# Kernel optimization log

Measured on AMD Instinct MI355X. Metric: run time of the kernel, lower is better.

## Reference

```python
import jax, jax.numpy as jnp
import numpy as np

B, S, H, UNITS = 32, 2048, 1024, 1024

def setup_inputs() -> dict:
    key = jax.random.key(0)
    ks = jax.random.split(key, 8)
    sc_h = 1.0 / np.sqrt(H)
    sc_u = 1.0 / np.sqrt(UNITS)
    return {
        "query": jax.random.normal(ks[0], (B, H), jnp.float32),
        "values": jax.random.normal(ks[1], (B, S, H), jnp.float32),
        "W1": jax.random.normal(ks[2], (H, UNITS), jnp.float32) * sc_h,
        "b1": jnp.zeros((UNITS,), jnp.float32),
        "W2": jax.random.normal(ks[3], (H, UNITS), jnp.float32) * sc_h,
        "b2": jnp.zeros((UNITS,), jnp.float32),
        "V": jax.random.normal(ks[4], (UNITS, 1), jnp.float32) * sc_u,
        "bv": jnp.zeros((1,), jnp.float32),
    }

def reference(query, values, W1, b1, W2, b2, V, bv):
    # W1(values): [B,S,U]; W2(query)[:,None,:]: [B,1,U] broadcast-added
    proj = jnp.tanh(
        jnp.einsum("bsh,hu->bsu", values, W1) + b1
        + (query @ W2 + b2)[:, None, :]
    )
    score = proj @ V + bv                      # [B,S,1]
    attention_weights = jax.nn.softmax(score, axis=1)  # softmax over seq
    context_vector = jnp.sum(attention_weights * values, axis=1)  # [B,H]
    return context_vector, attention_weights
```

## Files before the change

### kernel.cpp

```cpp
#include <hip/hip_runtime.h>
#include <hip/hip_bf16.h>


#define B_ 32
#define S_ 2048
#define H_ 1024
#define U_ 1024
#define M_ (B_ * S_)

typedef __bf16 bf16;
typedef __bf16 bf16x8 __attribute__((ext_vector_type(8)));
typedef __bf16 bf16x4 __attribute__((ext_vector_type(4)));
typedef float  f32x4  __attribute__((ext_vector_type(4)));

__device__ __forceinline__ void gl2lds16(const void* g, void* l) {
    __builtin_amdgcn_global_load_lds(
        (const __attribute__((address_space(1))) void*)g,
        (__attribute__((address_space(3))) void*)l, 16, 0, 0);
}

__global__ void cast_values(const float* __restrict__ in, bf16* __restrict__ out) {
    long i = ((long)blockIdx.x * 256 + threadIdx.x) * 8;
    float4 f0 = *reinterpret_cast<const float4*>(in + i);
    float4 f1 = *reinterpret_cast<const float4*>(in + i + 4);
    bf16x8 o;
    o[0] = (bf16)f0.x; o[1] = (bf16)f0.y; o[2] = (bf16)f0.z; o[3] = (bf16)f0.w;
    o[4] = (bf16)f1.x; o[5] = (bf16)f1.y; o[6] = (bf16)f1.z; o[7] = (bf16)f1.w;
    *reinterpret_cast<bf16x8*>(out + i) = o;
}

__global__ void transpose_w1(const float* __restrict__ W1, bf16* __restrict__ W1T) {
    __shared__ bf16 t[64 * 65];
    int h0 = blockIdx.x * 64, u0 = blockIdx.y * 64;
    int tid = threadIdx.x;
    #pragma unroll
    for (int i = 0; i < 16; ++i) {
        int idx = i * 256 + tid;
        int r = idx >> 6, c = idx & 63;
        t[c * 65 + r] = (bf16)W1[(long)(h0 + r) * U_ + u0 + c];
    }
    __syncthreads();
    #pragma unroll
    for (int i = 0; i < 16; ++i) {
        int idx = i * 256 + tid;
        int r = idx >> 6, c = idx & 63;
        W1T[(long)(u0 + r) * H_ + h0 + c] = t[r * 65 + c];
    }
}

__global__ void q2_kernel(const float* __restrict__ query, const float* __restrict__ W2,
                          const float* __restrict__ b2, float* __restrict__ q2) {
    __shared__ float qsh[H_];
    __shared__ float part[4][64];
    int b = blockIdx.y;
    int u0 = blockIdx.x * 64;
    int tid = threadIdx.x;
    int ul = tid & 63, kc = tid >> 6;
    for (int i = tid; i < H_; i += 256) qsh[i] = query[b * H_ + i];
    __syncthreads();
    float acc = 0.f;
    const float* wp = W2 + (long)(kc * 256) * U_ + u0 + ul;
    #pragma unroll 8
    for (int h = 0; h < 256; ++h) acc += qsh[kc * 256 + h] * wp[(long)h * U_];
    part[kc][ul] = acc;
    __syncthreads();
    if (tid < 64)
        q2[b * U_ + u0 + tid] = part[0][tid] + part[1][tid] + part[2][tid] + part[3][tid]
                                + b2[u0 + tid];
}

__global__ __launch_bounds__(256) void score_gemm(
    const bf16* __restrict__ A,
    const bf16* __restrict__ BT,
    const float* __restrict__ b1, const float* __restrict__ q2,
    const float* __restrict__ V, float* __restrict__ score )
{
    __shared__ __align__(16) bf16 a_sh[128 * 32];
    __shared__ __align__(16) bf16 b_sh[128 * 32];
    const int tid  = threadIdx.x;
    const int lane = tid & 63;
    const int wave = tid >> 6;
    const int wm = wave >> 1, wn = wave & 1;
    const int xcd = blockIdx.x & 7;
    const int i_  = blockIdx.x >> 3;
    const int nt  = i_ & 7;
    const int mt  = xcd * 64 + (i_ >> 3);
    const long m0 = (long)mt * 128;
    const int  n0 = nt * 128;
    const int lrow = lane & 15;
    const int quad = lane >> 4;

    f32x4 acc[4][4];
    const f32x4 zero = {0.f, 0.f, 0.f, 0.f};
    #pragma unroll
    for (int mi = 0; mi < 4; ++mi)
        #pragma unroll
        for (int ni = 0; ni < 4; ++ni) acc[mi][ni] = zero;

    const bf16* Abase = A + m0 * H_;
    const bf16* Bbase = BT + (long)n0 * H_;

    for (int kt = 0; kt < H_; kt += 32) {
        #pragma unroll
        for (int i = 0; i < 2; ++i) {
            int q = wave + i * 4;
            int c = (q << 6) + lane;
            int row = c >> 2, kp = c & 3;
            gl2lds16(Abase + (long)row * H_ + kt + kp * 8, (void*)(a_sh + (q << 9)));
            gl2lds16(Bbase + (long)row * H_ + kt + kp * 8, (void*)(b_sh + (q << 9)));
        }
        __syncthreads();

        bf16x8 af[4], bg[4];
        #pragma unroll
        for (int mi = 0; mi < 4; ++mi)
            af[mi] = *reinterpret_cast<const bf16x8*>(
                a_sh + ((wm * 64 + mi * 16 + lrow) * 32 + quad * 8));
        #pragma unroll
        for (int ni = 0; ni < 4; ++ni)
            bg[ni] = *reinterpret_cast<const bf16x8*>(
                b_sh + ((wn * 64 + ni * 16 + lrow) * 32 + quad * 8));

        #pragma unroll
        for (int mi = 0; mi < 4; ++mi)
            #pragma unroll
            for (int ni = 0; ni < 4; ++ni)
                acc[mi][ni] = __builtin_amdgcn_mfma_f32_16x16x32_bf16(
                    af[mi], bg[ni], acc[mi][ni], 0, 0, 0);
        __syncthreads();
    }

    const int bb = (int)(m0 / S_);
    float bq[4], vv[4];
    #pragma unroll
    for (int ni = 0; ni < 4; ++ni) {
        int u = n0 + wn * 64 + ni * 16 + lrow;
        bq[ni] = b1[u] + q2[bb * U_ + u];
        vv[ni] = V[u];
    }
    #pragma unroll
    for (int mi = 0; mi < 4; ++mi) {
        #pragma unroll
        for (int r = 0; r < 4; ++r) {
            float s = 0.f;
            #pragma unroll
            for (int ni = 0; ni < 4; ++ni) {
                float x = acc[mi][ni][r] + bq[ni];
                float t = 1.f - 2.f / (__expf(2.f * x) + 1.f);
                s += t * vv[ni];
            }
            s += __shfl_xor(s, 1); s += __shfl_xor(s, 2);
            s += __shfl_xor(s, 4); s += __shfl_xor(s, 8);
            if (lrow == 0)
                atomicAdd(score + m0 + wm * 64 + mi * 16 + quad * 4 + r, s);
        }
    }
}

__global__ void softmax_kernel(float* __restrict__ attn) {
    __shared__ float sh[S_];
    __shared__ float red[8];
    int b = blockIdx.x, tid = threadIdx.x;
    float* row = attn + (long)b * S_;
    float lmax = -1e30f;
    for (int i = tid; i < S_; i += 256) { float v = row[i]; sh[i] = v; lmax = fmaxf(lmax, v); }
    #pragma unroll
    for (int m = 32; m; m >>= 1) lmax = fmaxf(lmax, __shfl_xor(lmax, m));
    if ((tid & 63) == 0) red[tid >> 6] = lmax;
    __syncthreads();
    float gmax = fmaxf(fmaxf(red[0], red[1]), fmaxf(red[2], red[3]));
    float lsum = 0.f;
    for (int i = tid; i < S_; i += 256) { float e = __expf(sh[i] - gmax); sh[i] = e; lsum += e; }
    #pragma unroll
    for (int m = 32; m; m >>= 1) lsum += __shfl_xor(lsum, m);
    if ((tid & 63) == 0) red[4 + (tid >> 6)] = lsum;
    __syncthreads();
    float inv = 1.f / (red[4] + red[5] + red[6] + red[7]);
    for (int i = tid; i < S_; i += 256) row[i] = sh[i] * inv;
}

__global__ void context_kernel(const bf16* __restrict__ vals, const float* __restrict__ attn,
                               float* __restrict__ ctx ) {
    __shared__ float a_sh[128];
    int b = blockIdx.x >> 4;
    int sc = blockIdx.x & 15;
    int tid = threadIdx.x;
    if (tid < 128) a_sh[tid] = attn[(long)b * S_ + sc * 128 + tid];
    __syncthreads();
    const bf16* base = vals + ((long)b * S_ + sc * 128) * H_ + tid * 4;
    float ax = 0.f, ay = 0.f, az = 0.f, aw = 0.f;
    #pragma unroll 4
    for (int s = 0; s < 128; ++s) {
        float w = a_sh[s];
        bf16x4 v = *reinterpret_cast<const bf16x4*>(base + (long)s * H_);
        ax += w * (float)v[0]; ay += w * (float)v[1];
        az += w * (float)v[2]; aw += w * (float)v[3];
    }
    float* c = ctx + (long)b * H_ + tid * 4;
    atomicAdd(c + 0, ax); atomicAdd(c + 1, ay);
    atomicAdd(c + 2, az); atomicAdd(c + 3, aw);
}

extern "C" void kernel_launch(void* const* d_in, const int* in_sizes, int n_in,
                              void* d_out, int out_size, void* d_ws, size_t ws_size,
                              hipStream_t stream) {
    const float* query  = (const float*)d_in[0];
    const float* values = (const float*)d_in[1];
    const float* W1     = (const float*)d_in[2];
    const float* b1     = (const float*)d_in[3];
    const float* W2     = (const float*)d_in[4];
    const float* b2     = (const float*)d_in[5];
    const float* V      = (const float*)d_in[6];

    char* ws = (char*)d_ws;
    bf16*  vals_bf = (bf16*)ws;
    bf16*  w1t     = (bf16*)(ws + (size_t)M_ * H_ * 2);
    float* q2      = (float*)(ws + (size_t)M_ * H_ * 2 + (size_t)U_ * H_ * 2);

    float* ctx  = (float*)d_out;
    float* attn = (float*)d_out + B_ * H_;

    hipMemsetAsync(d_out, 0, (size_t)(B_ * H_ + B_ * S_) * sizeof(float), stream);

    cast_values  <<<(M_ * H_) / (256 * 8), 256, 0, stream>>>(values, vals_bf);
    transpose_w1 <<<dim3(16, 16),          256, 0, stream>>>(W1, w1t);
    q2_kernel    <<<dim3(U_ / 64, B_),     256, 0, stream>>>(query, W2, b2, q2);
    score_gemm   <<<(M_ / 128) * 8,        256, 0, stream>>>(vals_bf, w1t, b1, q2, V, attn);
    softmax_kernel<<<B_,                   256, 0, stream>>>(attn);
    context_kernel<<<B_ * 16,              256, 0, stream>>>(vals_bf, attn, ctx);
}
```

Before: 641.5 us.

## Fuse fp32-to-bf16 cast of values into score GEMM with swizzled LDS tiles

Removes the standalone cast kernel. The GEMM now loads fp32 values directly into swizzled LDS and converts them to bf16 in registers before MFMA. The blocks with nt==0 also write the bf16 copy needed by the context kernel. The K tile doubles to 64 and launch bounds request 3 blocks per CU. This trades a separate pass over values for twice the bytes of A per GEMM load and a larger LDS footprint.

Measured after the change: 616.0 us. 1.04x faster.

```diff
diff --git a/kernel.cpp b/kernel.cpp
--- a/kernel.cpp
+++ b/kernel.cpp
@@ -17,16 +17,6 @@
     __builtin_amdgcn_global_load_lds(
         (const __attribute__((address_space(1))) void*)g,
         (__attribute__((address_space(3))) void*)l, 16, 0, 0);
-}
-
-__global__ void cast_values(const float* __restrict__ in, bf16* __restrict__ out) {
-    long i = ((long)blockIdx.x * 256 + threadIdx.x) * 8;
-    float4 f0 = *reinterpret_cast<const float4*>(in + i);
-    float4 f1 = *reinterpret_cast<const float4*>(in + i + 4);
-    bf16x8 o;
-    o[0] = (bf16)f0.x; o[1] = (bf16)f0.y; o[2] = (bf16)f0.z; o[3] = (bf16)f0.w;
-    o[4] = (bf16)f1.x; o[5] = (bf16)f1.y; o[6] = (bf16)f1.z; o[7] = (bf16)f1.w;
-    *reinterpret_cast<bf16x8*>(out + i) = o;
 }
 
 __global__ void transpose_w1(const float* __restrict__ W1, bf16* __restrict__ W1T) {
@@ -69,14 +59,15 @@
                                 + b2[u0 + tid];
 }
 
-__global__ __launch_bounds__(256) void score_gemm(
-    const bf16* __restrict__ A,
+__global__ __launch_bounds__(256, 3) void score_gemm(
+    const float* __restrict__ A32,
     const bf16* __restrict__ BT,
     const float* __restrict__ b1, const float* __restrict__ q2,
-    const float* __restrict__ V, float* __restrict__ score )
+    const float* __restrict__ V, float* __restrict__ score ,
+    bf16* __restrict__ vals_bf)
 {
-    __shared__ __align__(16) bf16 a_sh[128 * 32];
-    __shared__ __align__(16) bf16 b_sh[128 * 32];
+    __shared__ __align__(16) float a_sh[2 * 128 * 32];
+    __shared__ __align__(16) bf16  b_sh[2 * 128 * 32];
     const int tid  = threadIdx.x;
     const int lane = tid & 63;
     const int wave = tid >> 6;
@@ -97,36 +88,80 @@
         #pragma unroll
         for (int ni = 0; ni < 4; ++ni) acc[mi][ni] = zero;
 
-    const bf16* Abase = A + m0 * H_;
-    const bf16* Bbase = BT + (long)n0 * H_;
-
-    for (int kt = 0; kt < H_; kt += 32) {
-        #pragma unroll
-        for (int i = 0; i < 2; ++i) {
-            int q = wave + i * 4;
-            int c = (q << 6) + lane;
-            int row = c >> 2, kp = c & 3;
-            gl2lds16(Abase + (long)row * H_ + kt + kp * 8, (void*)(a_sh + (q << 9)));
-            gl2lds16(Bbase + (long)row * H_ + kt + kp * 8, (void*)(b_sh + (q << 9)));
+    const float* Abase = A32 + m0 * H_;
+    const bf16*  Bbase = BT + (long)n0 * H_;
+
+    for (int kt = 0; kt < H_; kt += 64) {
+        #pragma unroll
+        for (int i = 0; i < 8; ++i) {
+            int g  = i * 4 + wave;
+            int hs = g >> 4, q = g & 15;
+            int row = q * 8 + (lane >> 3);
+            int gc  = (lane & 7) ^ (row & 7);
+            gl2lds16(Abase + (long)row * H_ + kt + hs * 32 + gc * 4,
+                     (void*)(a_sh + hs * 4096 + q * 256));
+        }
+        #pragma unroll
+        for (int i = 0; i < 4; ++i) {
+            int g  = i * 4 + wave;
+            int hs = g >> 3, q = g & 7;
+            int row = q * 16 + (lane >> 2);
+            int gc  = (lane & 3) ^ ((row >> 1) & 3);
+            gl2lds16(Bbase + (long)row * H_ + kt + hs * 32 + gc * 8,
+                     (void*)(b_sh + hs * 4096 + q * 512));
         }
         __syncthreads();
 
-        bf16x8 af[4], bg[4];
-        #pragma unroll
-        for (int mi = 0; mi < 4; ++mi)
-            af[mi] = *reinterpret_cast<const bf16x8*>(
-                a_sh + ((wm * 64 + mi * 16 + lrow) * 32 + quad * 8));
-        #pragma unroll
-        for (int ni = 0; ni < 4; ++ni)
-            bg[ni] = *reinterpret_cast<const bf16x8*>(
-                b_sh + ((wn * 64 + ni * 16 + lrow) * 32 + quad * 8));
-
-        #pragma unroll
-        for (int mi = 0; mi < 4; ++mi)
-            #pragma unroll
-            for (int ni = 0; ni < 4; ++ni)
-                acc[mi][ni] = __builtin_amdgcn_mfma_f32_16x16x32_bf16(
-                    af[mi], bg[ni], acc[mi][ni], 0, 0, 0);
+        #pragma unroll
+        for (int hs = 0; hs < 2; ++hs) {
+            bf16x8 af[4], bg[4];
+            #pragma unroll
+            for (int mi = 0; mi < 4; ++mi) {
+                int r  = wm * 64 + mi * 16 + lrow;
+                int p0 = (2 * quad) ^ (r & 7);
+                const float4 lo = *reinterpret_cast<const float4*>(
+                    a_sh + hs * 4096 + r * 32 + p0 * 4);
+                const float4 hi = *reinterpret_cast<const float4*>(
+                    a_sh + hs * 4096 + r * 32 + (p0 ^ 1) * 4);
+                bf16x8 f;
+                f[0] = (bf16)lo.x; f[1] = (bf16)lo.y; f[2] = (bf16)lo.z; f[3] = (bf16)lo.w;
+                f[4] = (bf16)hi.x; f[5] = (bf16)hi.y; f[6] = (bf16)hi.z; f[7] = (bf16)hi.w;
+                af[mi] = f;
+            }
+            #pragma unroll
+            for (int ni = 0; ni < 4; ++ni) {
+                int r = wn * 64 + ni * 16 + lrow;
+                int p = quad ^ ((r >> 1) & 3);
+                bg[ni] = *reinterpret_cast<const bf16x8*>(
+                    b_sh + hs * 4096 + r * 32 + p * 8);
+            }
+            #pragma unroll
+            for (int mi = 0; mi < 4; ++mi)
+                #pragma unroll
+                for (int ni = 0; ni < 4; ++ni)
+                    acc[mi][ni] = __builtin_amdgcn_mfma_f32_16x16x32_bf16(
+                        af[mi], bg[ni], acc[mi][ni], 0, 0, 0);
+        }
+
+        if (nt == 0) {
+            int row = tid >> 1, seg = tid & 1, s = row & 7;
+            #pragma unroll
+            for (int hs = 0; hs < 2; ++hs) {
+                float4 c[4];
+                #pragma unroll
+                for (int j = 0; j < 4; ++j)
+                    c[j] = *reinterpret_cast<const float4*>(
+                        a_sh + hs * 4096 + row * 32 + (((seg * 4 + j) ^ s) * 4));
+                bf16x8 o0, o1;
+                o0[0] = (bf16)c[0].x; o0[1] = (bf16)c[0].y; o0[2] = (bf16)c[0].z; o0[3] = (bf16)c[0].w;
+                o0[4] = (bf16)c[1].x; o0[5] = (bf16)c[1].y; o0[6] = (bf16)c[1].z; o0[7] = (bf16)c[1].w;
+                o1[0] = (bf16)c[2].x; o1[1] = (bf16)c[2].y; o1[2] = (bf16)c[2].z; o1[3] = (bf16)c[2].w;
+                o1[4] = (bf16)c[3].x; o1[5] = (bf16)c[3].y; o1[6] = (bf16)c[3].z; o1[7] = (bf16)c[3].w;
+                bf16* dst = vals_bf + (m0 + row) * H_ + kt + hs * 32 + seg * 16;
+                *reinterpret_cast<bf16x8*>(dst)     = o0;
+                *reinterpret_cast<bf16x8*>(dst + 8) = o1;
+            }
+        }
         __syncthreads();
     }
 
@@ -222,10 +257,9 @@
 
     hipMemsetAsync(d_out, 0, (size_t)(B_ * H_ + B_ * S_) * sizeof(float), stream);
 
-    cast_values  <<<(M_ * H_) / (256 * 8), 256, 0, stream>>>(values, vals_bf);
-    transpose_w1 <<<dim3(16, 16),          256, 0, stream>>>(W1, w1t);
-    q2_kernel    <<<dim3(U_ / 64, B_),     256, 0, stream>>>(query, W2, b2, q2);
-    score_gemm   <<<(M_ / 128) * 8,        256, 0, stream>>>(vals_bf, w1t, b1, q2, V, attn);
-    softmax_kernel<<<B_,                   256, 0, stream>>>(attn);
-    context_kernel<<<B_ * 16,              256, 0, stream>>>(vals_bf, attn, ctx);
-}
+    transpose_w1  <<<dim3(16, 16),       256, 0, stream>>>(W1, w1t);
+    q2_kernel     <<<dim3(U_ / 64, B_),  256, 0, stream>>>(query, W2, b2, q2);
+    score_gemm    <<<(M_ / 128) * 8,     256, 0, stream>>>(values, w1t, b1, q2, V, attn, vals_bf);
+    softmax_kernel<<<B_,                 256, 0, stream>>>(attn);
+    context_kernel<<<B_ * 16,            256, 0, stream>>>(vals_bf, attn, ctx);
+}
```
